# Kernel optimization log

Hardware: AMD Instinct MI355X
Metric: run time of the kernel (lower is better)

## Reference

```python
import jax, jax.numpy as jnp
import numpy as np

NEG = -1e9  # finite mask value (avoids NaN rows for fully-masked queries)


def setup_inputs() -> dict:
    key = jax.random.key(0)
    kq, kk, kv, ks = jax.random.split(key, 4)
    B, H, N, E = 4, 8, 2048, 64
    Q = jax.random.normal(kq, (B, H, N, E), dtype=jnp.float32)
    K = jax.random.normal(kk, (B, H, N, E), dtype=jnp.float32)
    V = jax.random.normal(kv, (B, H, N, E), dtype=jnp.float32)
    seqlens = jax.random.randint(ks, (B,), 1, N + 1, dtype=jnp.int32)
    return {"Q": Q, "K": K, "V": V, "seqlens": seqlens}


def reference(Q, K, V, seqlens):
    # SparTA SeqlenDynamicSparseAttention: per-batch masked attention.
    # scores = Q @ K^T (no 1/sqrt(E) scaling inside the kernel; Q/K are
    # assumed to be already-projected), softmax over keys < seqlen[b],
    # output zeroed for query rows >= seqlen[b].
    B, H, N, E = Q.shape
    pos = jnp.arange(N)
    valid = pos[None, :] < seqlens[:, None]  # [B, N] bool
    scores = jnp.einsum('bhqe,bhke->bhqk', Q, K)  # [B,H,N,N]
    scores = jnp.where(valid[:, None, None, :], scores, NEG)
    probs = jax.nn.softmax(scores, axis=-1)
    out = jnp.einsum('bhqk,bhke->bhqe', probs, V)  # [B,H,N,E]
    out = jnp.where(valid[:, None, :, None], out, 0.0)
    return out
```

## Files before the change

### kernel.cpp

```cpp
#include <hip/hip_runtime.h>

using f32x4  = __attribute__((ext_vector_type(4))) float;
using h16x2  = __attribute__((ext_vector_type(2))) _Float16;
using h16x4  = __attribute__((ext_vector_type(4))) _Float16;
using h16x8  = __attribute__((ext_vector_type(8))) _Float16;
using fp16x2 = __attribute__((ext_vector_type(2))) __fp16;

#define NEGBIG (-1e30f)
#define LOG2E  1.44269504f

constexpr int BH = 32, Nn = 2048, En = 64;

__device__ inline h16x8 cvt8(f32x4 x, f32x4 y) {
    union { h16x8 v; fp16x2 p[4]; } u;
    u.p[0] = __builtin_amdgcn_cvt_pkrtz(x[0], x[1]);
    u.p[1] = __builtin_amdgcn_cvt_pkrtz(x[2], x[3]);
    u.p[2] = __builtin_amdgcn_cvt_pkrtz(y[0], y[1]);
    u.p[3] = __builtin_amdgcn_cvt_pkrtz(y[2], y[3]);
    return u.v;
}
__device__ inline h16x4 cvt4(f32x4 x) {
    union { h16x4 v; fp16x2 p[2]; } u;
    u.p[0] = __builtin_amdgcn_cvt_pkrtz(x[0], x[1]);
    u.p[1] = __builtin_amdgcn_cvt_pkrtz(x[2], x[3]);
    return u.v;
}

__launch_bounds__(512)
__global__ void attn_part(const float* __restrict__ Qg,
                          const float* __restrict__ Kg,
                          const float* __restrict__ Vg,
                          const int*   __restrict__ seqlens,
                          _Float16*    __restrict__ Opart,
                          float*       __restrict__ Wpart,
                          int chunk)
{
    const int qblk = blockIdx.x;
    const int bh   = blockIdx.y;
    const int s    = blockIdx.z;
    const int seqlen = seqlens[bh >> 3];
    const int qstart = qblk * 128;
    const int kbeg   = s * chunk;
    if (qstart >= seqlen || kbeg >= seqlen) return;
    const int kend = min(seqlen, kbeg + chunk);

    const float* Qb = Qg + (size_t)bh * Nn * En;
    const float* Kb = Kg + (size_t)bh * Nn * En;
    const float* Vb = Vg + (size_t)bh * Nn * En;
    const int tid = threadIdx.x;

    __shared__ __attribute__((aligned(16))) _Float16 Ksh[64 * 64];
    __shared__ __attribute__((aligned(16))) _Float16 Vsh[64 * 64];

    const int wid  = tid >> 6;
    const int qsub = wid >> 2;
    const int widq = wid & 3;
    const int lane = tid & 63;
    const int lg   = lane >> 4;
    const int l16  = lane & 15;
    const bool active = (qstart + qsub * 64) < seqlen;

    const int qrow = qstart + qsub * 64 + widq * 16 + l16;
    h16x8 Qf[2];
    #pragma unroll
    for (int es = 0; es < 2; ++es) {
        const f32x4* qp = (const f32x4*)(Qb + (size_t)qrow * En + es * 32 + lg * 8);
        f32x4 x = qp[0] * LOG2E, y = qp[1] * LOG2E;
        Qf[es] = cvt8(x, y);
    }

    const int rK   = tid >> 3;
    const int cK   = tid & 7;
    const int vkey = tid & 63;
    const int ve0  = (tid >> 6) * 8;

    float m = NEGBIG, L = 0.f;
    f32x4 Ot[4] = {{0,0,0,0},{0,0,0,0},{0,0,0,0},{0,0,0,0}};

    auto loadStage = [&](int ks, f32x4& k0, f32x4& k1, f32x4& v0, f32x4& v1) {
        const f32x4* kp = (const f32x4*)(Kb + (size_t)(ks + rK) * En + cK * 8);
        k0 = kp[0]; k1 = kp[1];
        const f32x4* vp = (const f32x4*)(Vb + (size_t)(ks + vkey) * En + ve0);
        v0 = vp[0]; v1 = vp[1];
    };
    auto writeStage = [&](const f32x4& k0, const f32x4& k1,
                          const f32x4& v0, const f32x4& v1) {
        *(h16x8*)&Ksh[rK * 64 + ((cK ^ (rK & 7)) << 3)] = cvt8(k0, k1);
        float vv[8] = {v0[0], v0[1], v0[2], v0[3], v1[0], v1[1], v1[2], v1[3]};
        #pragma unroll
        for (int i = 0; i < 8; ++i) {
            int e = ve0 + i;
            Vsh[e * 64 + (((vkey >> 2) ^ (i << 1)) << 2) + (vkey & 3)] =
                (_Float16)vv[i];
        }
    };
    auto computeTile = [&](int ks) {
        if (!active) return;
        f32x4 St[4];
        #pragma unroll
        for (int kt = 0; kt < 4; ++kt) {
            f32x4 acc = {0, 0, 0, 0};
            int key = kt * 16 + l16;
            #pragma unroll
            for (int es = 0; es < 2; ++es) {
                int c = es * 4 + lg;
                h16x8 kf = *(const h16x8*)&Ksh[key * 64 + ((c ^ (key & 7)) << 3)];
                acc = __builtin_amdgcn_mfma_f32_16x16x32_f16(kf, Qf[es], acc, 0, 0, 0);
            }
            St[kt] = acc;
        }
        if (ks + 64 > seqlen) {
            #pragma unroll
            for (int kt = 0; kt < 4; ++kt) {
                int kb0 = ks + kt * 16 + lg * 4;
                #pragma unroll
                for (int j = 0; j < 4; ++j)
                    if (kb0 + j >= seqlen) St[kt][j] = NEGBIG;
            }
        }
        float tm = NEGBIG;
        #pragma unroll
        for (int kt = 0; kt < 4; ++kt)
            #pragma unroll
            for (int j = 0; j < 4; ++j) tm = fmaxf(tm, St[kt][j]);
        tm = fmaxf(tm, __shfl_xor(tm, 16));
        tm = fmaxf(tm, __shfl_xor(tm, 32));

        if (__any(tm > m + 8.f)) {
            float mn = fmaxf(m, tm);
            float sc = __builtin_amdgcn_exp2f(m - mn);
            m = mn; L *= sc;
            #pragma unroll
            for (int et = 0; et < 4; ++et) Ot[et] *= sc;
        }
        float ps = 0.f;
        h16x4 Pf[4];
        #pragma unroll
        for (int kt = 0; kt < 4; ++kt) {
            float p0 = __builtin_amdgcn_exp2f(St[kt][0] - m);
            float p1 = __builtin_amdgcn_exp2f(St[kt][1] - m);
            float p2 = __builtin_amdgcn_exp2f(St[kt][2] - m);
            float p3 = __builtin_amdgcn_exp2f(St[kt][3] - m);
            ps += (p0 + p1) + (p2 + p3);
            union { h16x4 v; fp16x2 p[2]; } u;
            u.p[0] = __builtin_amdgcn_cvt_pkrtz(p0, p1);
            u.p[1] = __builtin_amdgcn_cvt_pkrtz(p2, p3);
            Pf[kt] = u.v;
        }
        ps += __shfl_xor(ps, 16);
        ps += __shfl_xor(ps, 32);
        L += ps;
        #pragma unroll
        for (int kt = 0; kt < 4; ++kt) {
            #pragma unroll
            for (int et = 0; et < 4; ++et) {
                int e  = et * 16 + l16;
                int c8 = kt * 4 + lg;
                h16x4 vf = *(const h16x4*)&Vsh[e * 64 + ((c8 ^ ((e & 7) << 1)) << 2)];
                Ot[et] = __builtin_amdgcn_mfma_f32_16x16x16f16(vf, Pf[kt], Ot[et], 0, 0, 0);
            }
        }
    };

    f32x4 kA0, kA1, vA0, vA1, kB0, kB1, vB0, vB1;
    loadStage(kbeg, kA0, kA1, vA0, vA1);
    int ks = kbeg;
    while (true) {
        __syncthreads();
        writeStage(kA0, kA1, vA0, vA1);
        if (ks + 64 < kend) loadStage(ks + 64, kB0, kB1, vB0, vB1);
        __syncthreads();
        computeTile(ks);
        ks += 64;
        if (ks >= kend) break;

        __syncthreads();
        writeStage(kB0, kB1, vB0, vB1);
        if (ks + 64 < kend) loadStage(ks + 64, kA0, kA1, vA0, vA1);
        __syncthreads();
        computeTile(ks);
        ks += 64;
        if (ks >= kend) break;
    }

    if (active && qrow < seqlen) {
        float lw = m + __log2f(L);
        const size_t rbase = ((size_t)s * BH + bh) * Nn + qrow;
        if (lg == 0) Wpart[rbase] = lw;
        float invL = 1.f / L;
        _Float16* op = Opart + rbase * En;
        #pragma unroll
        for (int et = 0; et < 4; ++et) {
            f32x4 o = Ot[et] * invL;
            *(h16x4*)&op[et * 16 + lg * 4] = cvt4(o);
        }
    }
}

__launch_bounds__(256)
__global__ void reduce_k(const _Float16* __restrict__ Opart,
                         const float*    __restrict__ Wpart,
                         const int*      __restrict__ seqlens,
                         float*          __restrict__ Og,
                         int cshift)
{
    const int tid  = threadIdx.x;
    const int r    = tid >> 3;
    const int e8   = tid & 7;
    const int grow = blockIdx.x * 32 + r;
    const int bh   = grow >> 11;
    const int row  = grow & (Nn - 1);
    const int seqlen = seqlens[bh >> 3];

    f32x4 a0 = {0, 0, 0, 0}, a1 = {0, 0, 0, 0};
    if (row < seqlen) {
        const int chunk = 1 << cshift;
        const int nlive = (seqlen + chunk - 1) >> cshift;
        float W = NEGBIG;
        for (int s = 0; s < nlive; ++s)
            W = fmaxf(W, Wpart[((size_t)s * BH + bh) * Nn + row]);
        float denom = 0.f;
        for (int s = 0; s < nlive; ++s) {
            const size_t rbase = ((size_t)s * BH + bh) * Nn + row;
            float a = __builtin_amdgcn_exp2f(Wpart[rbase] - W);
            denom += a;
            h16x8 o = *(const h16x8*)&Opart[rbase * En + e8 * 8];
            a0[0] += a * (float)o[0]; a0[1] += a * (float)o[1];
            a0[2] += a * (float)o[2]; a0[3] += a * (float)o[3];
            a1[0] += a * (float)o[4]; a1[1] += a * (float)o[5];
            a1[2] += a * (float)o[6]; a1[3] += a * (float)o[7];
        }
        float sc = 1.f / denom;
        a0 *= sc; a1 *= sc;
    }
    float* op = Og + ((size_t)bh * Nn + row) * En + e8 * 8;
    *(f32x4*)op       = a0;
    *(f32x4*)(op + 4) = a1;
}

__launch_bounds__(512)
__global__ void attn_kernel(const float* __restrict__ Qg,
                            const float* __restrict__ Kg,
                            const float* __restrict__ Vg,
                            const int*   __restrict__ seqlens,
                            float*       __restrict__ Og)
{
    const int qblk = blockIdx.x;
    const int bh   = blockIdx.y;
    const int seqlen = seqlens[bh >> 3];
    const int qstart = qblk * 128;
    const int tid = threadIdx.x;
    float* Ob = Og + ((size_t)bh * Nn + qstart) * En;
    if (qstart >= seqlen) {
        f32x4 z = {0.f, 0.f, 0.f, 0.f};
        f32x4* op = (f32x4*)Ob;
        #pragma unroll
        for (int i = 0; i < 4; ++i) op[tid + i * 512] = z;
        return;
    }
    const float* Qb = Qg + (size_t)bh * Nn * En;
    const float* Kb = Kg + (size_t)bh * Nn * En;
    const float* Vb = Vg + (size_t)bh * Nn * En;
    __shared__ __attribute__((aligned(16))) _Float16 Ksh[64 * 64];
    __shared__ __attribute__((aligned(16))) _Float16 Vsh[64 * 64];
    const int wid  = tid >> 6;
    const int qsub = wid >> 2;
    const int widq = wid & 3;
    const int lane = tid & 63;
    const int lg   = lane >> 4;
    const int l16  = lane & 15;
    const bool active = (qstart + qsub * 64) < seqlen;
    const int qrow = qstart + qsub * 64 + widq * 16 + l16;
    h16x8 Qf[2];
    #pragma unroll
    for (int es = 0; es < 2; ++es) {
        const f32x4* qp = (const f32x4*)(Qb + (size_t)qrow * En + es * 32 + lg * 8);
        f32x4 x = qp[0] * LOG2E, y = qp[1] * LOG2E;
        Qf[es] = cvt8(x, y);
    }
    const int rK = tid >> 3, cK = tid & 7, vkey = tid & 63, ve0 = (tid >> 6) * 8;
    float m = NEGBIG, L = 0.f;
    f32x4 Ot[4] = {{0,0,0,0},{0,0,0,0},{0,0,0,0},{0,0,0,0}};
    auto loadStage = [&](int ks, f32x4& k0, f32x4& k1, f32x4& v0, f32x4& v1) {
        const f32x4* kp = (const f32x4*)(Kb + (size_t)(ks + rK) * En + cK * 8);
        k0 = kp[0]; k1 = kp[1];
        const f32x4* vp = (const f32x4*)(Vb + (size_t)(ks + vkey) * En + ve0);
        v0 = vp[0]; v1 = vp[1];
    };
    auto writeStage = [&](const f32x4& k0, const f32x4& k1,
                          const f32x4& v0, const f32x4& v1) {
        *(h16x8*)&Ksh[rK * 64 + ((cK ^ (rK & 7)) << 3)] = cvt8(k0, k1);
        float vv[8] = {v0[0], v0[1], v0[2], v0[3], v1[0], v1[1], v1[2], v1[3]};
        #pragma unroll
        for (int i = 0; i < 8; ++i) {
            int e = ve0 + i;
            Vsh[e * 64 + (((vkey >> 2) ^ (i << 1)) << 2) + (vkey & 3)] =
                (_Float16)vv[i];
        }
    };
    auto computeTile = [&](int ks) {
        if (!active) return;
        f32x4 St[4];
        #pragma unroll
        for (int kt = 0; kt < 4; ++kt) {
            f32x4 acc = {0, 0, 0, 0};
            int key = kt * 16 + l16;
            #pragma unroll
            for (int es = 0; es < 2; ++es) {
                int c = es * 4 + lg;
                h16x8 kf = *(const h16x8*)&Ksh[key * 64 + ((c ^ (key & 7)) << 3)];
                acc = __builtin_amdgcn_mfma_f32_16x16x32_f16(kf, Qf[es], acc, 0, 0, 0);
            }
            St[kt] = acc;
        }
        if (ks + 64 > seqlen) {
            #pragma unroll
            for (int kt = 0; kt < 4; ++kt) {
                int kb0 = ks + kt * 16 + lg * 4;
                #pragma unroll
                for (int j = 0; j < 4; ++j)
                    if (kb0 + j >= seqlen) St[kt][j] = NEGBIG;
            }
        }
        float tm = NEGBIG;
        #pragma unroll
        for (int kt = 0; kt < 4; ++kt)
            #pragma unroll
            for (int j = 0; j < 4; ++j) tm = fmaxf(tm, St[kt][j]);
        tm = fmaxf(tm, __shfl_xor(tm, 16));
        tm = fmaxf(tm, __shfl_xor(tm, 32));
        if (__any(tm > m + 8.f)) {
            float mn = fmaxf(m, tm);
            float sc = __builtin_amdgcn_exp2f(m - mn);
            m = mn; L *= sc;
            #pragma unroll
            for (int et = 0; et < 4; ++et) Ot[et] *= sc;
        }
        float ps = 0.f;
        h16x4 Pf[4];
        #pragma unroll
        for (int kt = 0; kt < 4; ++kt) {
            float p0 = __builtin_amdgcn_exp2f(St[kt][0] - m);
            float p1 = __builtin_amdgcn_exp2f(St[kt][1] - m);
            float p2 = __builtin_amdgcn_exp2f(St[kt][2] - m);
            float p3 = __builtin_amdgcn_exp2f(St[kt][3] - m);
            ps += (p0 + p1) + (p2 + p3);
            union { h16x4 v; fp16x2 p[2]; } u;
            u.p[0] = __builtin_amdgcn_cvt_pkrtz(p0, p1);
            u.p[1] = __builtin_amdgcn_cvt_pkrtz(p2, p3);
            Pf[kt] = u.v;
        }
        ps += __shfl_xor(ps, 16);
        ps += __shfl_xor(ps, 32);
        L += ps;
        #pragma unroll
        for (int kt = 0; kt < 4; ++kt) {
            #pragma unroll
            for (int et = 0; et < 4; ++et) {
                int e  = et * 16 + l16;
                int c8 = kt * 4 + lg;
                h16x4 vf = *(const h16x4*)&Vsh[e * 64 + ((c8 ^ ((e & 7) << 1)) << 2)];
                Ot[et] = __builtin_amdgcn_mfma_f32_16x16x16f16(vf, Pf[kt], Ot[et], 0, 0, 0);
            }
        }
    };
    f32x4 kA0, kA1, vA0, vA1, kB0, kB1, vB0, vB1;
    loadStage(0, kA0, kA1, vA0, vA1);
    int ks = 0;
    while (true) {
        __syncthreads();
        writeStage(kA0, kA1, vA0, vA1);
        if (ks + 64 < seqlen) loadStage(ks + 64, kB0, kB1, vB0, vB1);
        __syncthreads();
        computeTile(ks);
        ks += 64;
        if (ks >= seqlen) break;
        __syncthreads();
        writeStage(kB0, kB1, vB0, vB1);
        if (ks + 64 < seqlen) loadStage(ks + 64, kA0, kA1, vA0, vA1);
        __syncthreads();
        computeTile(ks);
        ks += 64;
        if (ks >= seqlen) break;
    }
    float invL = 1.f / L;
    float* orow = Ob + (size_t)(qsub * 64 + widq * 16 + l16) * En;
    if (qrow < seqlen) {
        #pragma unroll
        for (int et = 0; et < 4; ++et) {
            f32x4 o = Ot[et] * invL;
            *(f32x4*)(orow + et * 16 + lg * 4) = o;
        }
    } else {
        f32x4 z = {0, 0, 0, 0};
        #pragma unroll
        for (int et = 0; et < 4; ++et)
            *(f32x4*)(orow + et * 16 + lg * 4) = z;
    }
}

extern "C" void kernel_launch(void* const* d_in, const int* in_sizes, int n_in,
                              void* d_out, int out_size, void* d_ws, size_t ws_size,
                              hipStream_t stream)
{
    const float* Q  = (const float*)d_in[0];
    const float* K  = (const float*)d_in[1];
    const float* V  = (const float*)d_in[2];
    const int*   SL = (const int*)d_in[3];
    float*       O  = (float*)d_out;

    auto need = [](int S) {
        return (size_t)S * BH * Nn * En * sizeof(_Float16)
             + (size_t)S * BH * Nn * sizeof(float);
    };
    int S = 0;
    if      (ws_size >= need(4)) S = 4;
    else if (ws_size >= need(2)) S = 2;

    if (S) {
        _Float16* Opart = (_Float16*)d_ws;
        float*    Wpart = (float*)((char*)d_ws
                            + (size_t)S * BH * Nn * En * sizeof(_Float16));
        const int chunk  = Nn / S;
        const int cshift = (S == 4) ? 9 : 10;
        attn_part<<<dim3(Nn / 128, BH, S), 512, 0, stream>>>(
            Q, K, V, SL, Opart, Wpart, chunk);
        reduce_k<<<dim3(BH * Nn / 32), 256, 0, stream>>>(
            Opart, Wpart, SL, O, cshift);
    } else {
        attn_kernel<<<dim3(Nn / 128, BH), 512, 0, stream>>>(Q, K, V, SL, O);
    }
}
```

Baseline: 136.3 us.

## Switch attention partial kernel to 32x32x16 MFMA with double-buffered LDS

Rewrites the split-K attention kernel so that each of four waves handles 32 query rows using 32x32x16 f16 MFMAs instead of 16x16 tiles. The P operand is rebuilt with cross-half-wave shuffles so it can feed the PV MFMA directly. K/V shared tiles are now double-buffered, which leaves a single barrier per tile instead of two. The block shrinks to 256 threads with launch bounds of 3 blocks per CU. This cuts LDS reads per FLOP and synchronisation cost, in exchange for higher register pressure from the 16-wide accumulators and extra shuffles.

Result: faster. 132.6 us (-2.8%).

```diff
diff --git a/kernel.cpp b/kernel.cpp
--- a/kernel.cpp
+++ b/kernel.cpp
@@ -1,6 +1,7 @@
 #include <hip/hip_runtime.h>
 
 using f32x4  = __attribute__((ext_vector_type(4))) float;
+using f32x16 = __attribute__((ext_vector_type(16))) float;
 using h16x2  = __attribute__((ext_vector_type(2))) _Float16;
 using h16x4  = __attribute__((ext_vector_type(4))) _Float16;
 using h16x8  = __attribute__((ext_vector_type(8))) _Float16;
@@ -25,8 +26,15 @@
     u.p[1] = __builtin_amdgcn_cvt_pkrtz(x[2], x[3]);
     return u.v;
 }
-
-__launch_bounds__(512)
+__device__ inline fp16x2 shfl32(fp16x2 x) {
+    union { fp16x2 h; int i; } u; u.h = x;
+    u.i = __shfl_xor(u.i, 32);
+    return u.h;
+}
+
+#define TILE_BARRIER() asm volatile("s_waitcnt lgkmcnt(0)\ns_barrier" ::: "memory")
+
+__launch_bounds__(256, 3)
 __global__ void attn_part(const float* __restrict__ Qg,
                           const float* __restrict__ Kg,
                           const float* __restrict__ Vg,
@@ -49,150 +57,172 @@
     const float* Vb = Vg + (size_t)bh * Nn * En;
     const int tid = threadIdx.x;
 
-    __shared__ __attribute__((aligned(16))) _Float16 Ksh[64 * 64];
-    __shared__ __attribute__((aligned(16))) _Float16 Vsh[64 * 64];
+    __shared__ __attribute__((aligned(16))) _Float16 Ksh[2][64 * 64];
+    __shared__ __attribute__((aligned(16))) _Float16 Vsh[2][64 * 64];
 
     const int wid  = tid >> 6;
-    const int qsub = wid >> 2;
-    const int widq = wid & 3;
     const int lane = tid & 63;
-    const int lg   = lane >> 4;
-    const int l16  = lane & 15;
-    const bool active = (qstart + qsub * 64) < seqlen;
-
-    const int qrow = qstart + qsub * 64 + widq * 16 + l16;
-    h16x8 Qf[2];
+    const int l31  = lane & 31;
+    const int h    = lane >> 5;
+
+    const int qbase = qstart + wid * 32;
+    const bool active = qbase < seqlen;
+    const int qrow = qbase + l31;
+
+    h16x8 Qf[4];
     #pragma unroll
-    for (int es = 0; es < 2; ++es) {
-        const f32x4* qp = (const f32x4*)(Qb + (size_t)qrow * En + es * 32 + lg * 8);
+    for (int es = 0; es < 4; ++es) {
+        const f32x4* qp = (const f32x4*)(Qb + (size_t)qrow * En + es * 16 + h * 8);
         f32x4 x = qp[0] * LOG2E, y = qp[1] * LOG2E;
         Qf[es] = cvt8(x, y);
     }
 
-    const int rK   = tid >> 3;
-    const int cK   = tid & 7;
     const int vkey = tid & 63;
-    const int ve0  = (tid >> 6) * 8;
-
+    const int vw   = tid >> 6;
+
+    const f32x16 z16 = {0,0,0,0,0,0,0,0,0,0,0,0,0,0,0,0};
     float m = NEGBIG, L = 0.f;
-    f32x4 Ot[4] = {{0,0,0,0},{0,0,0,0},{0,0,0,0},{0,0,0,0}};
-
-    auto loadStage = [&](int ks, f32x4& k0, f32x4& k1, f32x4& v0, f32x4& v1) {
-        const f32x4* kp = (const f32x4*)(Kb + (size_t)(ks + rK) * En + cK * 8);
-        k0 = kp[0]; k1 = kp[1];
-        const f32x4* vp = (const f32x4*)(Vb + (size_t)(ks + vkey) * En + ve0);
-        v0 = vp[0]; v1 = vp[1];
-    };
-    auto writeStage = [&](const f32x4& k0, const f32x4& k1,
-                          const f32x4& v0, const f32x4& v1) {
-        *(h16x8*)&Ksh[rK * 64 + ((cK ^ (rK & 7)) << 3)] = cvt8(k0, k1);
-        float vv[8] = {v0[0], v0[1], v0[2], v0[3], v1[0], v1[1], v1[2], v1[3]};
-        #pragma unroll
-        for (int i = 0; i < 8; ++i) {
-            int e = ve0 + i;
-            Vsh[e * 64 + (((vkey >> 2) ^ (i << 1)) << 2) + (vkey & 3)] =
-                (_Float16)vv[i];
-        }
-    };
-    auto computeTile = [&](int ks) {
+    f32x16 Ot[2] = {z16, z16};
+
+    f32x4 kr[2][2], vr[2][2];
+
+    auto loadStage = [&](int ks) {
+        #pragma unroll
+        for (int it = 0; it < 2; ++it) {
+            int cid = tid + 256 * it;
+            int r = cid >> 3, c = cid & 7;
+            const f32x4* kp = (const f32x4*)(Kb + (size_t)(ks + r) * En + c * 8);
+            kr[it][0] = kp[0]; kr[it][1] = kp[1];
+            const f32x4* vp = (const f32x4*)(Vb + (size_t)(ks + vkey) * En + vw * 8 + 32 * it);
+            vr[it][0] = vp[0]; vr[it][1] = vp[1];
+        }
+    };
+
+    auto writeStage = [&](int db) {
+        #pragma unroll
+        for (int it = 0; it < 2; ++it) {
+            int cid = tid + 256 * it;
+            int r = cid >> 3, c = cid & 7;
+            *(h16x8*)&Ksh[db][r * 64 + ((c ^ (r & 7)) << 3)] = cvt8(kr[it][0], kr[it][1]);
+            int e0 = vw * 8 + 32 * it;
+            float vv[8] = {vr[it][0][0], vr[it][0][1], vr[it][0][2], vr[it][0][3],
+                           vr[it][1][0], vr[it][1][1], vr[it][1][2], vr[it][1][3]};
+            #pragma unroll
+            for (int i = 0; i < 8; ++i) {
+                int e = e0 + i;
+                Vsh[db][e * 64 + (((vkey >> 2) ^ (i << 1)) << 2) + (vkey & 3)] =
+                    (_Float16)vv[i];
+            }
+        }
+    };
+
+    auto computeTile = [&](int db, int ks) {
         if (!active) return;
-        f32x4 St[4];
-        #pragma unroll
-        for (int kt = 0; kt < 4; ++kt) {
-            f32x4 acc = {0, 0, 0, 0};
-            int key = kt * 16 + l16;
-            #pragma unroll
-            for (int es = 0; es < 2; ++es) {
-                int c = es * 4 + lg;
-                h16x8 kf = *(const h16x8*)&Ksh[key * 64 + ((c ^ (key & 7)) << 3)];
-                acc = __builtin_amdgcn_mfma_f32_16x16x32_f16(kf, Qf[es], acc, 0, 0, 0);
+        const _Float16* Kl = Ksh[db];
+        const _Float16* Vl = Vsh[db];
+
+        f32x16 St[2];
+        #pragma unroll
+        for (int kt = 0; kt < 2; ++kt) {
+            f32x16 acc = z16;
+            #pragma unroll
+            for (int es = 0; es < 4; ++es) {
+                h16x8 kf = *(const h16x8*)
+                    &Kl[(32 * kt + l31) * 64 + ((((es << 1) + h) ^ (l31 & 7)) << 3)];
+                acc = __builtin_amdgcn_mfma_f32_32x32x16_f16(kf, Qf[es], acc, 0, 0, 0);
             }
             St[kt] = acc;
         }
         if (ks + 64 > seqlen) {
             #pragma unroll
-            for (int kt = 0; kt < 4; ++kt) {
-                int kb0 = ks + kt * 16 + lg * 4;
+            for (int kt = 0; kt < 2; ++kt) {
                 #pragma unroll
-                for (int j = 0; j < 4; ++j)
-                    if (kb0 + j >= seqlen) St[kt][j] = NEGBIG;
-            }
-        }
-        float tm = NEGBIG;
-        #pragma unroll
-        for (int kt = 0; kt < 4; ++kt)
-            #pragma unroll
-            for (int j = 0; j < 4; ++j) tm = fmaxf(tm, St[kt][j]);
-        tm = fmaxf(tm, __shfl_xor(tm, 16));
+                for (int r = 0; r < 16; ++r) {
+                    int key = ks + 32 * kt + 4 * h + ((r & 3) + 8 * (r >> 2));
+                    if (key >= seqlen) St[kt][r] = NEGBIG;
+                }
+            }
+        }
+
+        float tm = St[0][0];
+        #pragma unroll
+        for (int r = 1; r < 16; ++r) tm = fmaxf(tm, St[0][r]);
+        #pragma unroll
+        for (int r = 0; r < 16; ++r) tm = fmaxf(tm, St[1][r]);
         tm = fmaxf(tm, __shfl_xor(tm, 32));
 
         if (__any(tm > m + 8.f)) {
             float mn = fmaxf(m, tm);
             float sc = __builtin_amdgcn_exp2f(m - mn);
             m = mn; L *= sc;
-            #pragma unroll
-            for (int et = 0; et < 4; ++et) Ot[et] *= sc;
-        }
+            Ot[0] *= sc; Ot[1] *= sc;
+        }
+
         float ps = 0.f;
-        h16x4 Pf[4];
-        #pragma unroll
-        for (int kt = 0; kt < 4; ++kt) {
-            float p0 = __builtin_amdgcn_exp2f(St[kt][0] - m);
-            float p1 = __builtin_amdgcn_exp2f(St[kt][1] - m);
-            float p2 = __builtin_amdgcn_exp2f(St[kt][2] - m);
-            float p3 = __builtin_amdgcn_exp2f(St[kt][3] - m);
-            ps += (p0 + p1) + (p2 + p3);
-            union { h16x4 v; fp16x2 p[2]; } u;
-            u.p[0] = __builtin_amdgcn_cvt_pkrtz(p0, p1);
-            u.p[1] = __builtin_amdgcn_cvt_pkrtz(p2, p3);
-            Pf[kt] = u.v;
-        }
-        ps += __shfl_xor(ps, 16);
+        fp16x2 pk[2][8];
+        #pragma unroll
+        for (int kt = 0; kt < 2; ++kt) {
+            #pragma unroll
+            for (int mm = 0; mm < 8; ++mm) {
+                float p0 = __builtin_amdgcn_exp2f(St[kt][2 * mm]     - m);
+                float p1 = __builtin_amdgcn_exp2f(St[kt][2 * mm + 1] - m);
+                ps += p0 + p1;
+                pk[kt][mm] = __builtin_amdgcn_cvt_pkrtz(p0, p1);
+            }
+        }
         ps += __shfl_xor(ps, 32);
         L += ps;
-        #pragma unroll
-        for (int kt = 0; kt < 4; ++kt) {
-            #pragma unroll
-            for (int et = 0; et < 4; ++et) {
-                int e  = et * 16 + l16;
-                int c8 = kt * 4 + lg;
-                h16x4 vf = *(const h16x4*)&Vsh[e * 64 + ((c8 ^ ((e & 7) << 1)) << 2)];
-                Ot[et] = __builtin_amdgcn_mfma_f32_16x16x16f16(vf, Pf[kt], Ot[et], 0, 0, 0);
-            }
-        }
-    };
-
-    f32x4 kA0, kA1, vA0, vA1, kB0, kB1, vB0, vB1;
-    loadStage(kbeg, kA0, kA1, vA0, vA1);
-    int ks = kbeg;
+
+        #pragma unroll
+        for (int kstep = 0; kstep < 4; ++kstep) {
+            const int kt = kstep >> 1, k4 = (kstep & 1) * 4;
+            fp16x2 sendA = h ? pk[kt][k4 + 0] : pk[kt][k4 + 2];
+            fp16x2 sendB = h ? pk[kt][k4 + 1] : pk[kt][k4 + 3];
+            fp16x2 recvA = shfl32(sendA);
+            fp16x2 recvB = shfl32(sendB);
+            fp16x2 ownLo = h ? pk[kt][k4 + 2] : pk[kt][k4 + 0];
+            fp16x2 ownHi = h ? pk[kt][k4 + 3] : pk[kt][k4 + 1];
+            union { h16x8 v; fp16x2 d[4]; } pf;
+            pf.d[0] = h ? recvA : ownLo;
+            pf.d[1] = h ? recvB : ownHi;
+            pf.d[2] = h ? ownLo : recvA;
+            pf.d[3] = h ? ownHi : recvB;
+            #pragma unroll
+            for (int et = 0; et < 2; ++et) {
+                h16x8 vf = *(const h16x8*)
+                    &Vl[(32 * et + l31) * 64 +
+                        ((((kstep << 2) + (h << 1)) ^ ((l31 & 7) << 1)) << 2)];
+                Ot[et] = __builtin_amdgcn_mfma_f32_32x32x16_f16(vf, pf.v, Ot[et], 0, 0, 0);
+            }
+        }
+    };
+
+    int ks = kbeg, db = 0;
+    loadStage(ks);
     while (true) {
-        __syncthreads();
-        writeStage(kA0, kA1, vA0, vA1);
-        if (ks + 64 < kend) loadStage(ks + 64, kB0, kB1, vB0, vB1);
-        __syncthreads();
-        computeTile(ks);
+        writeStage(db);
+        if (ks + 64 < kend) loadStage(ks + 64);
+        TILE_BARRIER();
+        computeTile(db, ks);
         ks += 64;
         if (ks >= kend) break;
-
-        __syncthreads();
-        writeStage(kB0, kB1, vB0, vB1);
-        if (ks + 64 < kend) loadStage(ks + 64, kA0, kA1, vA0, vA1);
-        __syncthreads();
-        computeTile(ks);
-        ks += 64;
-        if (ks >= kend) break;
+        db ^= 1;
     }
 
     if (active && qrow < seqlen) {
         float lw = m + __log2f(L);
         const size_t rbase = ((size_t)s * BH + bh) * Nn + qrow;
-        if (lg == 0) Wpart[rbase] = lw;
+        if (h == 0) Wpart[rbase] = lw;
         float invL = 1.f / L;
         _Float16* op = Opart + rbase * En;
         #pragma unroll
-        for (int et = 0; et < 4; ++et) {
-            f32x4 o = Ot[et] * invL;
-            *(h16x4*)&op[et * 16 + lg * 4] = cvt4(o);
+        for (int et = 0; et < 2; ++et) {
+            #pragma unroll
+            for (int r1 = 0; r1 < 4; ++r1) {
+                f32x4 o = {Ot[et][4 * r1 + 0] * invL, Ot[et][4 * r1 + 1] * invL,
+                           Ot[et][4 * r1 + 2] * invL, Ot[et][4 * r1 + 3] * invL};
+                *(h16x4*)&op[et * 32 + r1 * 8 + h * 4] = cvt4(o);
+            }
         }
     }
 }
@@ -423,7 +453,7 @@
                             + (size_t)S * BH * Nn * En * sizeof(_Float16));
         const int chunk  = Nn / S;
         const int cshift = (S == 4) ? 9 : 10;
-        attn_part<<<dim3(Nn / 128, BH, S), 512, 0, stream>>>(
+        attn_part<<<dim3(Nn / 128, BH, S), 256, 0, stream>>>(
             Q, K, V, SL, Opart, Wpart, chunk);
         reduce_k<<<dim3(BH * Nn / 32), 256, 0, stream>>>(
             Opart, Wpart, SL, O, cshift);
```
